# Optimization experiments

Measured on AMD Instinct MI355X. Metric: run time of the kernel, lower is better.

Reference implementation:

```python
import jax, jax.numpy as jnp
import numpy as np
from jax.scipy import special

B, N, DIM, H, DK, DV, F = 2, 1536, 1536, 8, 64, 64, 192


def _pos_embed(seq_len, feat):
    """Enformer relative positional basis: [2*seq_len-1, feat]."""
    per = feat // 6  # 3 basis families x (symmetric, antisymmetric)
    d = jnp.arange(-seq_len + 1, seq_len, dtype=jnp.float32)
    ad = jnp.abs(d)[:, None]  # [2N-1, 1]
    # exponential decay, log-spaced half lives
    half_life = 2.0 ** jnp.linspace(3.0, float(np.log2(seq_len)), per)
    expo = jnp.exp(-jnp.log(2.0) / half_life * ad)
    # central binary mask
    widths = 2.0 ** jnp.arange(1, per + 1, dtype=jnp.float32) - 1.0
    cmask = (widths > ad).astype(jnp.float32)
    # gamma pdf basis
    stddev = seq_len / (2.0 * per)
    start_mean = seq_len / per
    mean = jnp.linspace(start_mean, float(seq_len), per)
    conc = (mean / stddev) ** 2
    rate = mean / stddev ** 2
    log_unnorm = special.xlogy(conc - 1.0, ad) - rate * ad
    log_norm = special.gammaln(conc) - conc * jnp.log(rate)
    probs = jnp.exp(log_unnorm - log_norm) + 1e-8
    gamma = probs / jnp.max(probs, axis=-1, keepdims=True)
    emb = jnp.concatenate([expo, cmask, gamma], axis=-1)
    emb = jnp.concatenate([emb, jnp.sign(d)[:, None] * emb], axis=-1)
    return emb.astype(jnp.float32)


def _relative_shift(x):
    # x: [B, H, N, 2N-1] -> [B, H, N, N] (Transformer-XL shift)
    b, h, t1, t2 = x.shape
    x = jnp.pad(x, ((0, 0), (0, 0), (0, 0), (1, 0)))  # [B,H,N,2N]
    x = x.reshape(b, h, t2 + 1, t1)[:, :, 1:, :].reshape(b, h, t1, t2)
    return x[..., : (t2 + 2) // 2]


def setup_inputs() -> dict:
    key = jax.random.key(0)
    ks = jax.random.split(key, 8)
    s = 0.02
    return {
        "x": jax.random.normal(ks[0], (B, N, DIM), dtype=jnp.float32),
        "Wq": jax.random.normal(ks[1], (DIM, H * DK), dtype=jnp.float32) * s,
        "Wk": jax.random.normal(ks[2], (DIM, H * DK), dtype=jnp.float32) * s,
        "Wv": jax.random.normal(ks[3], (DIM, H * DV), dtype=jnp.float32) * s,
        "Wrel": jax.random.normal(ks[4], (F, H * DK), dtype=jnp.float32) * s,
        "Wout": jax.random.normal(ks[5], (H * DV, DIM), dtype=jnp.float32) * s,
        "bout": jnp.zeros((DIM,), dtype=jnp.float32),
        "rel_content_bias": jax.random.normal(ks[6], (1, H, 1, DK), dtype=jnp.float32),
        "rel_pos_bias": jax.random.normal(ks[7], (1, H, 1, DK), dtype=jnp.float32),
        "pos_embed": _pos_embed(N, F),  # [2N-1, F] buffer
    }


def reference(x, Wq, Wk, Wv, Wrel, Wout, bout, rel_content_bias, rel_pos_bias, pos_embed):
    b, n, _ = x.shape
    h, dk = rel_content_bias.shape[1], rel_content_bias.shape[3]
    dv = Wv.shape[1] // h
    scale = dk ** -0.5
    q = (x @ Wq).reshape(b, n, h, dk).transpose(0, 2, 1, 3) * scale  # [b,h,n,dk]
    k = (x @ Wk).reshape(b, n, h, dk).transpose(0, 2, 1, 3)
    v = (x @ Wv).reshape(b, n, h, dv).transpose(0, 2, 1, 3)
    content_logits = jnp.einsum('bhid,bhjd->bhij', q + rel_content_bias, k)
    rel_k = (pos_embed @ Wrel).reshape(-1, h, dk).transpose(1, 0, 2)  # [h,2n-1,dk]
    rel_logits = jnp.einsum('bhid,hjd->bhij', q + rel_pos_bias, rel_k)  # [b,h,n,2n-1]
    rel_logits = _relative_shift(rel_logits)  # [b,h,n,n]
    attn = jax.nn.softmax(content_logits + rel_logits, axis=-1)
    out = jnp.einsum('bhij,bhjd->bhid', attn, v)
    out = out.transpose(0, 2, 1, 3).reshape(b, n, h * dv)
    return out @ Wout + bout
```

## Files before the change

### kernel.cpp

```cpp
#include <hip/hip_runtime.h>

#define NSEQ  1536
#define HEADS 8
#define NREL  3071
#define NRELP 3072

typedef __bf16 bf16;
typedef __bf16 bf16x8 __attribute__((ext_vector_type(8)));
typedef __bf16 bf16x4 __attribute__((ext_vector_type(4)));
typedef float  f32x4  __attribute__((ext_vector_type(4)));

static __device__ __forceinline__ f32x4 mfma16(bf16x8 a, bf16x8 b, f32x4 c) {
  return __builtin_amdgcn_mfma_f32_16x16x32_bf16(a, b, c, 0, 0, 0);
}

static __device__ __forceinline__ void gload_lds16(const bf16* g, bf16* l) {
  __builtin_amdgcn_global_load_lds((const __attribute__((address_space(1))) void*)g,
                                   (__attribute__((address_space(3))) void*)l, 16, 0, 0);
}

#define DPP_F(v, ctrl) __int_as_float(__builtin_amdgcn_update_dpp(0, __float_as_int(v), ctrl, 0xF, 0xF, true))
static __device__ __forceinline__ float rowsum16(float v) {
  v += DPP_F(v, 0xB1);
  v += DPP_F(v, 0x4E);
  v += DPP_F(v, 0x124);
  v += DPP_F(v, 0x128);
  return v;
}

__global__ __launch_bounds__(256) void prep(const float* __restrict__ x, const float* __restrict__ pos,
                                            const float* __restrict__ Wq, const float* __restrict__ Wk,
                                            const float* __restrict__ Wv, const float* __restrict__ Wout,
                                            const float* __restrict__ Wrel,
                                            bf16* __restrict__ xb, bf16* __restrict__ posb,
                                            bf16* __restrict__ WT, bf16* __restrict__ WoT,
                                            bf16* __restrict__ WrT) {
  int blk = blockIdx.x;
  if (blk < 4608) {
    int i = blk * 256 + threadIdx.x;
    float4 v = ((const float4*)x)[i];
    bf16x4 o;
    o[0] = (bf16)v.x; o[1] = (bf16)v.y; o[2] = (bf16)v.z; o[3] = (bf16)v.w;
    ((bf16x4*)xb)[i] = o;
    return;
  }
  blk -= 4608;
  if (blk < 576) {
    int i = blk * 256 + threadIdx.x;
    if (i < (NREL * 192 / 4)) {
      float4 v = ((const float4*)pos)[i];
      bf16x4 o;
      o[0] = (bf16)v.x; o[1] = (bf16)v.y; o[2] = (bf16)v.z; o[3] = (bf16)v.w;
      ((bf16x4*)posb)[i] = o;
    }
    return;
  }
  blk -= 576;
  const float* in; bf16* out; int C, ostride, orowoff, cx, ry;
  if (blk < 768)       { in = Wq;   out = WT;  C = 512;  ostride = 1536; orowoff = 0;    cx = blk % 16; ry = blk / 16; }
  else if (blk < 1536) { blk -= 768;  in = Wk;   out = WT;  C = 512;  ostride = 1536; orowoff = 512;  cx = blk % 16; ry = blk / 16; }
  else if (blk < 2304) { blk -= 1536; in = Wv;   out = WT;  C = 512;  ostride = 1536; orowoff = 1024; cx = blk % 16; ry = blk / 16; }
  else if (blk < 3072) { blk -= 2304; in = Wout; out = WoT; C = 1536; ostride = 512;  orowoff = 0;    cx = blk % 48; ry = blk / 48; }
  else                 { blk -= 3072; in = Wrel; out = WrT; C = 512;  ostride = 192;  orowoff = 0;    cx = blk % 16; ry = blk / 16; }
  __shared__ float t[32][33];
  int tx = threadIdx.x & 31, ty = threadIdx.x >> 5;
  int r0 = ry * 32, c0 = cx * 32;
#pragma unroll
  for (int i = 0; i < 4; i++)
    t[ty + 8 * i][tx] = in[(size_t)(r0 + ty + 8 * i) * C + c0 + tx];
  __syncthreads();
#pragma unroll
  for (int i = 0; i < 4; i++)
    out[(size_t)(c0 + ty + 8 * i + orowoff) * ostride + r0 + tx] = (bf16)t[tx][ty + 8 * i];
}

static __device__ __forceinline__ void gemm_core(const bf16* __restrict__ A, const bf16* __restrict__ BT,
                                                 int Klen, int ldk, int m0, int n0, int M,
                                                 bf16* sa, bf16* sb, f32x4 acc[4][2]) {
  int tid = threadIdx.x, wave = tid >> 6, lane = tid & 63;
  int l15 = lane & 15, quad = lane >> 4;
  int lrow = lane >> 3, lcg = lane & 7;
  int swz = (lcg ^ lrow) * 8;

  int rowA = wave * 16 + lrow;
  int ra0 = m0 + rowA;     if (ra0 > M - 1) ra0 = M - 1;
  int ra1 = m0 + rowA + 8; if (ra1 > M - 1) ra1 = M - 1;
  const bf16* pA0 = A + (size_t)ra0 * ldk + swz;
  const bf16* pA1 = A + (size_t)ra1 * ldk + swz;
  int rowB = wave * 32 + lrow;
  const bf16* pB = BT + (size_t)(n0 + rowB) * ldk + swz;
  size_t ldk8 = (size_t)ldk * 8;
  bf16* wA = sa + rowA * 64 + lcg * 8;
  bf16* wB = sb + rowB * 64 + lcg * 8;

  float4 a0 = *(const float4*)pA0;
  float4 a1 = *(const float4*)pA1;
  float4 b0 = *(const float4*)(pB);
  float4 b1 = *(const float4*)(pB + ldk8);
  float4 b2 = *(const float4*)(pB + 2 * ldk8);
  float4 b3 = *(const float4*)(pB + 3 * ldk8);

  int swzA = (quad ^ (l15 & 7)) * 8;
  int swzB = ((4 + quad) ^ (l15 & 7)) * 8;

  for (int k0 = 0; k0 < Klen; k0 += 64) {
    __syncthreads();
    *(float4*)(wA) = a0;        *(float4*)(wA + 512) = a1;
    *(float4*)(wB) = b0;        *(float4*)(wB + 512) = b1;
    *(float4*)(wB + 1024) = b2; *(float4*)(wB + 1536) = b3;
    __syncthreads();
    if (k0 + 64 < Klen) {
      pA0 += 64; pA1 += 64; pB += 64;
      a0 = *(const float4*)pA0;
      a1 = *(const float4*)pA1;
      b0 = *(const float4*)(pB);
      b1 = *(const float4*)(pB + ldk8);
      b2 = *(const float4*)(pB + 2 * ldk8);
      b3 = *(const float4*)(pB + 3 * ldk8);
    }
#pragma unroll
    for (int kq = 0; kq < 2; kq++) {
      bf16x8 af[4], bfr[2];
      int sz = kq ? swzB : swzA;
#pragma unroll
      for (int rt = 0; rt < 4; rt++)
        af[rt] = *(const bf16x8*)&sa[(rt * 16 + l15) * 64 + sz];
#pragma unroll
      for (int ct = 0; ct < 2; ct++)
        bfr[ct] = *(const bf16x8*)&sb[(wave * 32 + ct * 16 + l15) * 64 + sz];
#pragma unroll
      for (int ct = 0; ct < 2; ct++)
#pragma unroll
        for (int rt = 0; rt < 4; rt++)
          acc[rt][ct] = mfma16(af[rt], bfr[ct], acc[rt][ct]);
    }
  }
}

__global__ __launch_bounds__(256) void gemm_qkvrel(const bf16* __restrict__ xb, const bf16* __restrict__ WT,
                                                   const bf16* __restrict__ posb, const bf16* __restrict__ WrT,
                                                   const float* __restrict__ cb, const float* __restrict__ pb,
                                                   bf16* __restrict__ qc, bf16* __restrict__ qp,
                                                   bf16* __restrict__ kb, bf16* __restrict__ vt,
                                                   bf16* __restrict__ rk) {
  __shared__ __align__(16) bf16 sa[64 * 64];
  __shared__ __align__(16) bf16 sb[128 * 64];
  __shared__ __align__(16) bf16 tv[64 * 130];
  int tid = threadIdx.x, wave = tid >> 6, lane = tid & 63;
  int l15 = lane & 15, quad = lane >> 4;
  int m0 = blockIdx.x * 64;
  f32x4 acc[4][2] = {};
  if (blockIdx.y >= 12) {
    int n0 = (blockIdx.y - 12) * 128;
    gemm_core(posb, WrT, 192, 192, m0, n0, NREL, sa, sb, acc);
#pragma unroll
    for (int rt = 0; rt < 4; rt++)
#pragma unroll
      for (int ct = 0; ct < 2; ct++)
#pragma unroll
        for (int r = 0; r < 4; r++) {
          int row = m0 + rt * 16 + quad * 4 + r;
          if (row < NREL) {
            int col = n0 + wave * 32 + ct * 16 + l15;
            rk[((size_t)(col >> 6) * NRELP + row) * 64 + (col & 63)] = (bf16)acc[rt][ct][r];
          }
        }
    return;
  }
  int n0 = blockIdx.y * 128;
  gemm_core(xb, WT, 1536, 1536, m0, n0, 3072, sa, sb, acc);
  int b = m0 / NSEQ, nseq0 = m0 % NSEQ;
  if (blockIdx.y < 8) {
    bool isq = blockIdx.y < 4;
#pragma unroll
    for (int rt = 0; rt < 4; rt++)
#pragma unroll
      for (int ct = 0; ct < 2; ct++)
#pragma unroll
        for (int r = 0; r < 4; r++) {
          int row = nseq0 + rt * 16 + quad * 4 + r;
          int colg = n0 + wave * 32 + ct * 16 + l15;
          int col = colg & 511;
          int h = col >> 6, d = col & 63;
          size_t o = ((size_t)(b * 8 + h) * NSEQ + row) * 64 + d;
          float v = acc[rt][ct][r];
          if (isq) {
            float qv = v * 0.18033688011f;
            qc[o] = (bf16)(qv + cb[col] * 1.44269504089f);
            qp[o] = (bf16)(qv + pb[col] * 1.44269504089f);
          } else {
            kb[o] = (bf16)v;
          }
        }
  } else {
#pragma unroll
    for (int rt = 0; rt < 4; rt++)
#pragma unroll
      for (int ct = 0; ct < 2; ct++)
#pragma unroll
        for (int r = 0; r < 4; r++)
          tv[(rt * 16 + quad * 4 + r) * 130 + wave * 32 + ct * 16 + l15] = (bf16)acc[rt][ct][r];
    __syncthreads();
    int n = tid & 63, c0v = tid >> 6;
    int hbase = (blockIdx.y - 8) * 2;
#pragma unroll
    for (int hh = 0; hh < 2; hh++)
#pragma unroll
      for (int i = 0; i < 16; i++) {
        int dv = i * 4 + c0v;
        vt[((size_t)(b * 8 + hbase + hh) * 64 + dv) * NSEQ + nseq0 + n] = tv[n * 130 + hh * 64 + dv];
      }
  }
}

__global__ __launch_bounds__(256) void gemm_out(const bf16* __restrict__ A, const bf16* __restrict__ BT,
                                                float* __restrict__ C, const float* __restrict__ bias) {
  __shared__ __align__(16) bf16 sa[64 * 64];
  __shared__ __align__(16) bf16 sb[128 * 64];
  int tid = threadIdx.x, wave = tid >> 6, lane = tid & 63;
  int l15 = lane & 15, quad = lane >> 4;
  int m0 = blockIdx.x * 64, n0 = blockIdx.y * 128;
  f32x4 acc[4][2] = {};
  gemm_core(A, BT, 512, 512, m0, n0, 3072, sa, sb, acc);
#pragma unroll
  for (int rt = 0; rt < 4; rt++)
#pragma unroll
    for (int ct = 0; ct < 2; ct++)
#pragma unroll
      for (int r = 0; r < 4; r++) {
        int row = m0 + rt * 16 + quad * 4 + r;
        int col = n0 + wave * 32 + ct * 16 + l15;
        C[(size_t)row * 1536 + col] = acc[rt][ct][r] + bias[col];
      }
}

__global__ __launch_bounds__(256, 4) void attn(const bf16* __restrict__ qc, const bf16* __restrict__ qp,
                                               const bf16* __restrict__ kb, const bf16* __restrict__ vt,
                                               const bf16* __restrict__ rk,
                                               float* __restrict__ Opart, float* __restrict__ mlp) {
  __shared__ __align__(16) bf16 sk[64 * 64];
  __shared__ __align__(16) bf16 sv[64 * 64];
  __shared__ __align__(16) bf16 srel[128 * 64];
  __shared__ __align__(16) bf16 pls[4][16 * 64];
  int qb = blockIdx.x, bh = blockIdx.y, kz = blockIdx.z;
  int h = bh & 7;
  int i0 = qb * 64;
  int wave = threadIdx.x >> 6, lane = threadIdx.x & 63;
  int l15 = lane & 15, quad = lane >> 4;
  int lrow = lane >> 3, lcg = lane & 7;
  const bf16* qcb = qc + (size_t)bh * NSEQ * 64;
  const bf16* qpb = qp + (size_t)bh * NSEQ * 64;
  const bf16* kbb = kb + (size_t)bh * NSEQ * 64;
  const bf16* vtb = vt + (size_t)bh * 64 * NSEQ;
  const bf16* rkh = rk + (size_t)h * NRELP * 64;
  bf16* plsw = pls[wave];

  int qrow = i0 + wave * 16 + l15;
  bf16x8 aqc0 = *(const bf16x8*)(qcb + (size_t)qrow * 64 + quad * 8);
  bf16x8 aqc1 = *(const bf16x8*)(qcb + (size_t)qrow * 64 + 32 + quad * 8);
  bf16x8 aqp0 = *(const bf16x8*)(qpb + (size_t)qrow * 64 + quad * 8);
  bf16x8 aqp1 = *(const bf16x8*)(qpb + (size_t)qrow * 64 + 32 + quad * 8);

  int bidx[4];
  bool hisel[4];
#pragma unroll
  for (int r = 0; r < 4; r++) {
    int rl = quad * 4 + r;
    bidx[r] = (quad * 16 + ((l15 + 15 - rl) & 15)) << 2;
    hisel[r] = l15 > rl;
  }

  int swz = (lcg ^ lrow) * 8;
  int jb = 23 + kz * 12 - qb;
  const bf16* pK = kbb + (size_t)(kz * 768 + wave * 16 + lrow) * 64 + swz;
  const bf16* pV = vtb + (size_t)(wave * 16 + lrow) * NSEQ + kz * 768 + swz;
  const bf16* pR = rkh + (size_t)(jb + 1) * 4096 + (size_t)(wave * 16 + lrow) * 64 + swz;
  bf16* wK = sk + (wave * 16 + lrow) * 64 + lcg * 8;
  bf16* wV = sv + (wave * 16 + lrow) * 64 + lcg * 8;
  int wRoff = (wave * 16 + lrow) * 64 + lcg * 8;

  {
    const bf16* pP = rkh + (size_t)jb * 4096 + (size_t)(wave * 16 + lrow) * 64 + swz;
    bf16* dP = srel + ((jb & 1) * 64 + wave * 16) * 64;
#pragma unroll
    for (int t = 0; t < 2; t++)
      gload_lds16(pP + t * 512, dP + t * 512);
  }
  float4 kr0 = *(const float4*)(pK), kr1 = *(const float4*)(pK + 512);             pK += 4096;
  float4 vr0 = *(const float4*)(pV), vr1 = *(const float4*)(pV + 8 * NSEQ);        pV += 64;
  float4 rr0 = *(const float4*)(pR), rr1 = *(const float4*)(pR + 512);             pR += 4096;
  int pxor = (jb & 1) << 6;

  int swzA = (quad ^ (l15 & 7)) * 8;
  int swzB = ((4 + quad) ^ (l15 & 7)) * 8;
  int rb0 = (3 - wave) * 16 + l15;
  int pxl = (l15 >> 1) << 3;
  const bf16* plr = plsw + l15 * 64;

  f32x4 acco[4] = {};
  float li[4] = {0.0f, 0.0f, 0.0f, 0.0f};

  for (int jt = 0; jt < 12; jt++) {
    __syncthreads();
    *(float4*)(wK) = kr0;        *(float4*)(wK + 512) = kr1;
    *(float4*)(wV) = vr0;        *(float4*)(wV + 512) = vr1;
    {
      bf16* wR = srel + (pxor ^ 64) * 64 + wRoff;
      *(float4*)(wR) = rr0;      *(float4*)(wR + 512) = rr1;
    }
    __syncthreads();
    if (jt < 11) {
      kr0 = *(const float4*)(pK); kr1 = *(const float4*)(pK + 512);        pK += 4096;
      vr0 = *(const float4*)(pV); vr1 = *(const float4*)(pV + 8 * NSEQ);   pV += 64;
      rr0 = *(const float4*)(pR); rr1 = *(const float4*)(pR + 512);        pR += 4096;
    }
    f32x4 s[4] = {};
#pragma unroll
    for (int c = 0; c < 4; c++) {
      const bf16* kp = sk + (c * 16 + l15) * 64;
      s[c] = mfma16(aqc0, *(const bf16x8*)(kp + swzA), s[c]);
      s[c] = mfma16(aqc1, *(const bf16x8*)(kp + swzB), s[c]);
    }
    f32x4 sb5[5];
#pragma unroll
    for (int cc = 0; cc < 5; cc++) {
      const bf16* rp = srel + ((rb0 + cc * 16) ^ pxor) * 64;
      f32x4 z = {};
      z = mfma16(aqp0, *(const bf16x8*)(rp + swzA), z);
      sb5[cc] = mfma16(aqp1, *(const bf16x8*)(rp + swzB), z);
    }
#pragma unroll
    for (int r = 0; r < 4; r++) {
      float bp[5];
#pragma unroll
      for (int cc = 0; cc < 5; cc++)
        bp[cc] = __int_as_float(__builtin_amdgcn_ds_bpermute(bidx[r], __float_as_int(sb5[cc][r])));
#pragma unroll
      for (int c = 0; c < 4; c++)
        s[c][r] += hisel[r] ? bp[c + 1] : bp[c];
    }
#pragma unroll
    for (int c = 0; c < 4; c++)
#pragma unroll
      for (int r = 0; r < 4; r++) {
        float p = __builtin_amdgcn_exp2f(s[c][r] - 11.5415603f);
        bf16 pbh = (bf16)p;
        li[r] += (float)pbh;
        int prow = quad * 4 + r;
        plsw[prow * 64 + ((c * 16 + l15) ^ ((prow >> 1) << 3))] = pbh;
      }
#pragma unroll
    for (int ks = 0; ks < 2; ks++) {
      bf16x8 ap = *(const bf16x8*)(plr + ((ks * 32 + quad * 8) ^ pxl));
#pragma unroll
      for (int c = 0; c < 4; c++) {
        const bf16* vp = sv + (c * 16 + l15) * 64;
        acco[c] = mfma16(ap, *(const bf16x8*)(vp + (ks ? swzB : swzA)), acco[c]);
      }
    }
    pxor ^= 64;
  }
#pragma unroll
  for (int r = 0; r < 4; r++)
    li[r] = rowsum16(li[r]);
  int qt16 = qb * 4 + wave;
  size_t pbase = ((size_t)(bh * 96 + qt16) * 2 + kz);
#pragma unroll
  for (int c = 0; c < 4; c++)
#pragma unroll
    for (int r = 0; r < 4; r++)
      Opart[pbase * 1024 + (quad * 4 + r) * 64 + c * 16 + l15] = acco[c][r];
  if (l15 == 0) {
#pragma unroll
    for (int r = 0; r < 4; r++)
      mlp[pbase * 16 + quad * 4 + r] = li[r];
  }
}

__global__ void attn_merge(const float* __restrict__ Opart, const float* __restrict__ mlp,
                           bf16* __restrict__ O) {
  int qt = blockIdx.x, bh = blockIdx.y;
  int b = bh >> 3, h = bh & 7;
  int col = threadIdx.x & 63, rg = threadIdx.x >> 6;
  size_t base = (size_t)(bh * 96 + qt) * 2;
#pragma unroll
  for (int rr = 0; rr < 4; rr++) {
    int row = rg * 4 + rr;
    float L = mlp[base * 16 + row] + mlp[(base + 1) * 16 + row];
    float v = Opart[base * 1024 + row * 64 + col] + Opart[(base + 1) * 1024 + row * 64 + col];
    O[((size_t)(b * NSEQ + qt * 16 + row) * 8 + h) * 64 + col] = (bf16)(v / L);
  }
}

extern "C" void kernel_launch(void* const* d_in, const int* in_sizes, int n_in,
                              void* d_out, int out_size, void* d_ws, size_t ws_size,
                              hipStream_t stream) {
  const float* x    = (const float*)d_in[0];
  const float* Wq   = (const float*)d_in[1];
  const float* Wk   = (const float*)d_in[2];
  const float* Wv   = (const float*)d_in[3];
  const float* Wrel = (const float*)d_in[4];
  const float* Wout = (const float*)d_in[5];
  const float* bout = (const float*)d_in[6];
  const float* cb   = (const float*)d_in[7];
  const float* pb   = (const float*)d_in[8];
  const float* pos  = (const float*)d_in[9];
  float* out = (float*)d_out;

  char* ws = (char*)d_ws;
  size_t off = 0;
  auto alloc = [&](size_t bytes) {
    char* p = ws + off;
    off = (off + bytes + 255) & ~(size_t)255;
    return p;
  };
  bf16*  xb    = (bf16*)alloc(3072UL * 1536 * 2);
  bf16*  WT    = (bf16*)alloc(1536UL * 1536 * 2);
  bf16*  WoT   = (bf16*)alloc(1536UL * 512 * 2);
  bf16*  WrT   = (bf16*)alloc(512UL * 192 * 2);
  bf16*  posb  = (bf16*)alloc((size_t)NREL * 192 * 2);
  bf16*  qcb   = (bf16*)alloc(16UL * NSEQ * 64 * 2);
  bf16*  qpb   = (bf16*)alloc(16UL * NSEQ * 64 * 2);
  bf16*  kbb   = (bf16*)alloc(16UL * NSEQ * 64 * 2);
  bf16*  vtb   = (bf16*)alloc(16UL * NSEQ * 64 * 2);
  bf16*  rkb   = (bf16*)alloc(8UL * NRELP * 64 * 2);
  bf16*  Ob    = (bf16*)alloc(3072UL * 512 * 2);
  float* Opart = (float*)alloc(16UL * 96 * 2 * 1024 * 4);
  float* mlpw  = (float*)alloc(16UL * 96 * 2 * 16 * 4);

  prep<<<dim3(8352), 256, 0, stream>>>(x, pos, Wq, Wk, Wv, Wout, Wrel, xb, posb, WT, WoT, WrT);
  gemm_qkvrel<<<dim3(48, 16), 256, 0, stream>>>(xb, WT, posb, WrT, cb, pb, qcb, qpb, kbb, vtb, rkb);
  attn<<<dim3(24, 16, 2), 256, 0, stream>>>(qcb, qpb, kbb, vtb, rkb, Opart, mlpw);
  attn_merge<<<dim3(96, 16), 256, 0, stream>>>(Opart, mlpw, Ob);
  gemm_out<<<dim3(48, 12), 256, 0, stream>>>(Ob, WoT, out, bout);
}
```

Baseline: 174.4 us.

## Double-buffer GEMM tiles via direct global-to-LDS loads, remap attention blocks per XCD, add setprio

The shared GEMM core now stages A and B tiles with global_load_lds straight into double-buffered LDS. The next k-tile loads while the current one is consumed, so the register staging copy and one barrier per iteration go away. The attention kernel remaps its flat block index so blocks sharing a batch-head land on the same XCD for L2 reuse, and raises wave priority around the MFMA sections. LDS use doubles in the GEMMs, and the V-transpose buffer now aliases sb, which needs an extra barrier.

```diff
diff --git a/kernel.cpp b/kernel.cpp
--- a/kernel.cpp
+++ b/kernel.cpp
@@ -90,50 +90,52 @@
   int rowB = wave * 32 + lrow;
   const bf16* pB = BT + (size_t)(n0 + rowB) * ldk + swz;
   size_t ldk8 = (size_t)ldk * 8;
-  bf16* wA = sa + rowA * 64 + lcg * 8;
-  bf16* wB = sb + rowB * 64 + lcg * 8;
-
-  float4 a0 = *(const float4*)pA0;
-  float4 a1 = *(const float4*)pA1;
-  float4 b0 = *(const float4*)(pB);
-  float4 b1 = *(const float4*)(pB + ldk8);
-  float4 b2 = *(const float4*)(pB + 2 * ldk8);
-  float4 b3 = *(const float4*)(pB + 3 * ldk8);
 
   int swzA = (quad ^ (l15 & 7)) * 8;
   int swzB = ((4 + quad) ^ (l15 & 7)) * 8;
 
+  {
+    bf16* da = sa + (wave * 16) * 64;
+    gload_lds16(pA0, da);
+    gload_lds16(pA1, da + 512);
+    bf16* db = sb + (wave * 32) * 64;
+#pragma unroll
+    for (int t = 0; t < 4; t++)
+      gload_lds16(pB + t * ldk8, db + t * 512);
+  }
+
+  int bsel = 0;
   for (int k0 = 0; k0 < Klen; k0 += 64) {
     __syncthreads();
-    *(float4*)(wA) = a0;        *(float4*)(wA + 512) = a1;
-    *(float4*)(wB) = b0;        *(float4*)(wB + 512) = b1;
-    *(float4*)(wB + 1024) = b2; *(float4*)(wB + 1536) = b3;
-    __syncthreads();
     if (k0 + 64 < Klen) {
-      pA0 += 64; pA1 += 64; pB += 64;
-      a0 = *(const float4*)pA0;
-      a1 = *(const float4*)pA1;
-      b0 = *(const float4*)(pB);
-      b1 = *(const float4*)(pB + ldk8);
-      b2 = *(const float4*)(pB + 2 * ldk8);
-      b3 = *(const float4*)(pB + 3 * ldk8);
-    }
+      int nb = bsel ^ 1, koff = k0 + 64;
+      bf16* da = sa + nb * 4096 + (wave * 16) * 64;
+      gload_lds16(pA0 + koff, da);
+      gload_lds16(pA1 + koff, da + 512);
+      bf16* db = sb + nb * 8192 + (wave * 32) * 64;
+#pragma unroll
+      for (int t = 0; t < 4; t++)
+        gload_lds16(pB + koff + t * ldk8, db + t * 512);
+    }
+    const bf16* ca = sa + bsel * 4096;
+    const bf16* cbp = sb + bsel * 8192;
 #pragma unroll
     for (int kq = 0; kq < 2; kq++) {
       bf16x8 af[4], bfr[2];
       int sz = kq ? swzB : swzA;
 #pragma unroll
       for (int rt = 0; rt < 4; rt++)
-        af[rt] = *(const bf16x8*)&sa[(rt * 16 + l15) * 64 + sz];
+        af[rt] = *(const bf16x8*)&ca[(rt * 16 + l15) * 64 + sz];
 #pragma unroll
       for (int ct = 0; ct < 2; ct++)
-        bfr[ct] = *(const bf16x8*)&sb[(wave * 32 + ct * 16 + l15) * 64 + sz];
+        bfr[ct] = *(const bf16x8*)&cbp[(wave * 32 + ct * 16 + l15) * 64 + sz];
 #pragma unroll
       for (int ct = 0; ct < 2; ct++)
 #pragma unroll
         for (int rt = 0; rt < 4; rt++)
           acc[rt][ct] = mfma16(af[rt], bfr[ct], acc[rt][ct]);
     }
+    bsel ^= 1;
   }
 }
 
@@ -143,9 +145,9 @@
                                                    bf16* __restrict__ qc, bf16* __restrict__ qp,
                                                    bf16* __restrict__ kb, bf16* __restrict__ vt,
                                                    bf16* __restrict__ rk) {
-  __shared__ __align__(16) bf16 sa[64 * 64];
-  __shared__ __align__(16) bf16 sb[128 * 64];
-  __shared__ __align__(16) bf16 tv[64 * 130];
+  __shared__ __align__(16) bf16 sa[2 * 64 * 64];
+  __shared__ __align__(16) bf16 sb[2 * 128 * 64];
+  bf16* tv = sb;
   int tid = threadIdx.x, wave = tid >> 6, lane = tid & 63;
   int l15 = lane & 15, quad = lane >> 4;
   int m0 = blockIdx.x * 64;
@@ -193,6 +195,7 @@
           }
         }
   } else {
+    __syncthreads();
 #pragma unroll
     for (int rt = 0; rt < 4; rt++)
 #pragma unroll
@@ -215,8 +218,8 @@
 
 __global__ __launch_bounds__(256) void gemm_out(const bf16* __restrict__ A, const bf16* __restrict__ BT,
                                                 float* __restrict__ C, const float* __restrict__ bias) {
-  __shared__ __align__(16) bf16 sa[64 * 64];
-  __shared__ __align__(16) bf16 sb[128 * 64];
+  __shared__ __align__(16) bf16 sa[2 * 64 * 64];
+  __shared__ __align__(16) bf16 sb[2 * 128 * 64];
   int tid = threadIdx.x, wave = tid >> 6, lane = tid & 63;
   int l15 = lane & 15, quad = lane >> 4;
   int m0 = blockIdx.x * 64, n0 = blockIdx.y * 128;
@@ -242,7 +245,12 @@
   __shared__ __align__(16) bf16 sv[64 * 64];
   __shared__ __align__(16) bf16 srel[128 * 64];
   __shared__ __align__(16) bf16 pls[4][16 * 64];
-  int qb = blockIdx.x, bh = blockIdx.y, kz = blockIdx.z;
+  int flat = blockIdx.x + 24 * blockIdx.y + 384 * blockIdx.z;
+  int xcd = flat & 7, loc = flat >> 3;
+  int bh = (xcd << 1) + (loc >= 48 ? 1 : 0);
+  int rem = loc >= 48 ? loc - 48 : loc;
+  int kz = rem >= 24 ? 1 : 0;
+  int qb = rem - 24 * kz;
   int h = bh & 7;
   int i0 = qb * 64;
   int wave = threadIdx.x >> 6, lane = threadIdx.x & 63;
@@ -314,6 +322,7 @@
       vr0 = *(const float4*)(pV); vr1 = *(const float4*)(pV + 8 * NSEQ);   pV += 64;
       rr0 = *(const float4*)(pR); rr1 = *(const float4*)(pR + 512);        pR += 4096;
     }
+    __builtin_amdgcn_s_setprio(1);
     f32x4 s[4] = {};
 #pragma unroll
     for (int c = 0; c < 4; c++) {
@@ -329,6 +338,7 @@
       z = mfma16(aqp0, *(const bf16x8*)(rp + swzA), z);
       sb5[cc] = mfma16(aqp1, *(const bf16x8*)(rp + swzB), z);
     }
+    __builtin_amdgcn_s_setprio(0);
 #pragma unroll
     for (int r = 0; r < 4; r++) {
       float bp[5];
@@ -349,6 +359,7 @@
         int prow = quad * 4 + r;
         plsw[prow * 64 + ((c * 16 + l15) ^ ((prow >> 1) << 3))] = pbh;
       }
+    __builtin_amdgcn_s_setprio(1);
 #pragma unroll
     for (int ks = 0; ks < 2; ks++) {
       bf16x8 ap = *(const bf16x8*)(plr + ((ks * 32 + quad * 8) ^ pxl));
@@ -358,6 +369,7 @@
         acco[c] = mfma16(ap, *(const bf16x8*)(vp + (ks ? swzB : swzA)), acco[c]);
       }
     }
+    __builtin_amdgcn_s_setprio(0);
     pxor ^= 64;
   }
 #pragma unroll
```

After: 193.2 us. +10.7%, slower.
